# Kernel optimization log

Hardware: AMD Instinct MI355X
Metric: run time of the kernel (lower is better)

Reference implementation:

```python
import jax, jax.numpy as jnp
import numpy as np

B = 8192          # number of ragged samples (lengths.numel())
T = 1048576       # total tokens = sum(lengths), static for jit
NTOKEN = 100000
NHID = 256
NCLASSES = 14


def setup_inputs() -> dict:
    key = jax.random.key(0)
    k1, k2, k3, k4, k5 = jax.random.split(key, 5)
    # ragged lengths summing exactly to T: diff of sorted cut points
    cuts = jnp.sort(jax.random.randint(k1, (B - 1,), 0, T))
    bounds = jnp.concatenate([jnp.array([0], dtype=cuts.dtype), cuts,
                              jnp.array([T], dtype=cuts.dtype)])
    lengths = (bounds[1:] - bounds[:-1]).astype(jnp.int64)  # [B], may contain 0
    indices = jax.random.randint(k2, (T,), 0, NTOKEN).astype(jnp.int64)
    emb = jax.random.normal(k3, (NTOKEN, NHID), dtype=jnp.float32)
    W = jax.random.normal(k4, (NHID, NCLASSES), dtype=jnp.float32) / jnp.sqrt(jnp.float32(NHID))
    b = jax.random.normal(k5, (NCLASSES,), dtype=jnp.float32) * 0.01
    return {"lengths": lengths, "indices": indices, "emb": emb, "W": W, "b": b}


def reference(lengths, indices, emb, W, b):
    # segment id for each flat token: sample i owns lengths[i] consecutive tokens
    seg = jnp.repeat(jnp.arange(B), lengths, total_repeat_length=T)  # [T]
    gathered = emb[indices]                                          # [T, NHID]
    sums = jax.ops.segment_sum(gathered, seg, num_segments=B)       # [B, NHID]
    len_f = lengths.astype(sums.dtype)[:, None]                      # [B, 1]
    means = jnp.where(len_f > 0, sums / jnp.maximum(len_f, 1), 0.0)  # zero rows for empty samples
    return jnp.tanh(means) @ W + b                                   # [B, NCLASSES]
```

## Files before the change

kernel.cpp:

```cpp
#include <hip/hip_runtime.h>

#define B_SAMPLES 8192
#define NHID 256
#define NCLASSES 14
#define T_TOKENS 1048576
#define CHUNK 128
#define NWAVES (T_TOKENS / CHUNK)
#define NTOKEN_ROWS 100000
#define LMIN 40
#define SUMS_OFFSET 65536
#define SUMS_BYTES ((size_t)B_SAMPLES * NHID * 4)
#define EMB8_OFFSET (SUMS_OFFSET + SUMS_BYTES)
#define EMB8_BYTES ((size_t)NTOKEN_ROWS * NHID)
#define CONV_BLOCKS ((NTOKEN_ROWS * NHID) / (16 * 256))

__global__ __launch_bounds__(256) void scan_convert_kernel(
    const int* __restrict__ lengths, int* __restrict__ bounds,
    const float* __restrict__ emb, unsigned* __restrict__ emb8)
{
    if (blockIdx.x == 0) {
        __shared__ int s_sum[256];
        const int t = threadIdx.x;
        int local[32];
        int sum = 0;
#pragma unroll
        for (int k = 0; k < 32; ++k) {
            int v = lengths[t * 32 + k];
            local[k] = v;
            sum += v;
        }
        s_sum[t] = sum;
        __syncthreads();
        for (int off = 1; off < 256; off <<= 1) {
            int v = (t >= off) ? s_sum[t - off] : 0;
            __syncthreads();
            s_sum[t] += v;
            __syncthreads();
        }
        int run = (t > 0) ? s_sum[t - 1] : 0;
#pragma unroll
        for (int k = 0; k < 32; ++k) {
            bounds[t * 32 + k] = run;
            run += local[k];
        }
        if (t == 255) bounds[B_SAMPLES] = run;
    } else {
        const size_t i = ((size_t)(blockIdx.x - 1) * 256 + threadIdx.x) * 16;
        const float4 a = *reinterpret_cast<const float4*>(emb + i);
        const float4 b = *reinterpret_cast<const float4*>(emb + i + 4);
        const float4 c = *reinterpret_cast<const float4*>(emb + i + 8);
        const float4 d = *reinterpret_cast<const float4*>(emb + i + 12);
        uint4 o;
        int w;
        w = __builtin_amdgcn_cvt_pk_fp8_f32(a.x, a.y, 0, false);
        w = __builtin_amdgcn_cvt_pk_fp8_f32(a.z, a.w, w, true);
        o.x = (unsigned)w;
        w = __builtin_amdgcn_cvt_pk_fp8_f32(b.x, b.y, 0, false);
        w = __builtin_amdgcn_cvt_pk_fp8_f32(b.z, b.w, w, true);
        o.y = (unsigned)w;
        w = __builtin_amdgcn_cvt_pk_fp8_f32(c.x, c.y, 0, false);
        w = __builtin_amdgcn_cvt_pk_fp8_f32(c.z, c.w, w, true);
        o.z = (unsigned)w;
        w = __builtin_amdgcn_cvt_pk_fp8_f32(d.x, d.y, 0, false);
        w = __builtin_amdgcn_cvt_pk_fp8_f32(d.z, d.w, w, true);
        o.w = (unsigned)w;
        *reinterpret_cast<uint4*>(emb8 + i / 4) = o;
    }
}

#define FLUSH_ACC()                                                          \
    {                                                                        \
        float* dst_ = sums + (size_t)s * NHID + lane * 4;                    \
        if (inter) {                                                         \
            *reinterpret_cast<float4*>(dst_) = make_float4(ax, ay, az, aw);  \
        } else {                                                             \
            unsafeAtomicAdd(dst_ + 0, ax);                                   \
            unsafeAtomicAdd(dst_ + 1, ay);                                   \
            unsafeAtomicAdd(dst_ + 2, az);                                   \
            unsafeAtomicAdd(dst_ + 3, aw);                                   \
        }                                                                    \
    }

#define ACCUM(V, T_)                                                         \
    {                                                                        \
        if ((T_) == se) {                                                    \
            FLUSH_ACC();                                                     \
            ax = ay = az = aw = 0.f;                                         \
            ++s;                                                             \
            while (bounds[s + 1] <= (T_)) ++s;                               \
            se = bounds[s + 1];                                              \
            inter = (bounds[s] >= t0) && (se <= t1);                         \
        }                                                                    \
        {                                                                    \
            auto lo_ = __builtin_amdgcn_cvt_pk_f32_fp8((int)(V), false);     \
            auto hi_ = __builtin_amdgcn_cvt_pk_f32_fp8((int)(V), true);      \
            ax += lo_[0];                                                    \
            ay += lo_[1];                                                    \
            az += hi_[0];                                                    \
            aw += hi_[1];                                                    \
        }                                                                    \
    }

__global__ __launch_bounds__(256) void chunk_gather_fp8_kernel(
    const int* __restrict__ indices,
    const unsigned* __restrict__ emb8,
    const int* __restrict__ bounds,
    float* __restrict__ sums)
{
    const int wave = blockIdx.x * 4 + (threadIdx.x >> 6);
    const int lane = threadIdx.x & 63;
    const int t0 = wave * CHUNK;
    const int t1 = t0 + CHUNK;

    int lo = 0, hi = B_SAMPLES - 1;
    while (lo < hi) {
        const int mid = (lo + hi) >> 1;
        if (bounds[mid + 1] > t0) hi = mid; else lo = mid + 1;
    }
    int s = lo;
    int se = bounds[s + 1];
    bool inter = (bounds[s] >= t0) && (se <= t1);

    float ax = 0.f, ay = 0.f, az = 0.f, aw = 0.f;
    const int* ip = indices + t0;
    int4 ca = *reinterpret_cast<const int4*>(ip);
    int4 cb = *reinterpret_cast<const int4*>(ip + 4);

    for (int g = 0; g < CHUNK / 8; ++g) {
        int4 na = ca, nb = cb;
        if (g + 1 < CHUNK / 8) {
            na = *reinterpret_cast<const int4*>(ip + 8);
            nb = *reinterpret_cast<const int4*>(ip + 12);
        }
        ip += 8;
        const unsigned v0 = emb8[(size_t)(unsigned)ca.x * (NHID / 4) + lane];
        const unsigned v1 = emb8[(size_t)(unsigned)ca.y * (NHID / 4) + lane];
        const unsigned v2 = emb8[(size_t)(unsigned)ca.z * (NHID / 4) + lane];
        const unsigned v3 = emb8[(size_t)(unsigned)ca.w * (NHID / 4) + lane];
        const unsigned v4 = emb8[(size_t)(unsigned)cb.x * (NHID / 4) + lane];
        const unsigned v5 = emb8[(size_t)(unsigned)cb.y * (NHID / 4) + lane];
        const unsigned v6 = emb8[(size_t)(unsigned)cb.z * (NHID / 4) + lane];
        const unsigned v7 = emb8[(size_t)(unsigned)cb.w * (NHID / 4) + lane];

        const int tb = t0 + g * 8;
        ACCUM(v0, tb + 0)
        ACCUM(v1, tb + 1)
        ACCUM(v2, tb + 2)
        ACCUM(v3, tb + 3)
        ACCUM(v4, tb + 4)
        ACCUM(v5, tb + 5)
        ACCUM(v6, tb + 6)
        ACCUM(v7, tb + 7)
        ca = na;
        cb = nb;
    }
    FLUSH_ACC();
}

__global__ __launch_bounds__(256, 8) void head_kernel(
    const float* __restrict__ sums,
    const int* __restrict__ bounds,
    const int* __restrict__ indices,
    const float* __restrict__ emb,
    const float* __restrict__ W,
    const float* __restrict__ bias,
    float* __restrict__ out)
{
    const int s = blockIdx.x * 4 + (threadIdx.x >> 6);
    const int lane = threadIdx.x & 63;
    const int start = bounds[s];
    const int len = bounds[s + 1] - start;

    float ax, ay, az, aw;
    if (len >= LMIN) {
        const float4 v = *reinterpret_cast<const float4*>(sums + (size_t)s * NHID + lane * 4);
        ax = v.x; ay = v.y; az = v.z; aw = v.w;
    } else {
        ax = ay = az = aw = 0.f;
        const int* ip = indices + start;
        int j = 0;
        for (; j + 4 <= len; j += 4) {
            const int r0 = ip[j + 0];
            const int r1 = ip[j + 1];
            const int r2 = ip[j + 2];
            const int r3 = ip[j + 3];
            const float4 v0 = *reinterpret_cast<const float4*>(emb + (size_t)r0 * NHID + lane * 4);
            const float4 v1 = *reinterpret_cast<const float4*>(emb + (size_t)r1 * NHID + lane * 4);
            const float4 v2 = *reinterpret_cast<const float4*>(emb + (size_t)r2 * NHID + lane * 4);
            const float4 v3 = *reinterpret_cast<const float4*>(emb + (size_t)r3 * NHID + lane * 4);
            ax += (v0.x + v1.x) + (v2.x + v3.x);
            ay += (v0.y + v1.y) + (v2.y + v3.y);
            az += (v0.z + v1.z) + (v2.z + v3.z);
            aw += (v0.w + v1.w) + (v2.w + v3.w);
        }
        for (; j < len; ++j) {
            const int r = ip[j];
            const float4 v = *reinterpret_cast<const float4*>(emb + (size_t)r * NHID + lane * 4);
            ax += v.x; ay += v.y; az += v.z; aw += v.w;
        }
    }

    const float inv = (len > 0) ? 1.f / (float)len : 0.f;
    float th[4];
    th[0] = tanhf(ax * inv);
    th[1] = tanhf(ay * inv);
    th[2] = tanhf(az * inv);
    th[3] = tanhf(aw * inv);

    float p[NCLASSES];
#pragma unroll
    for (int c = 0; c < NCLASSES; ++c) p[c] = 0.f;
#pragma unroll
    for (int k = 0; k < 4; ++k) {
        const float* wr = W + (size_t)(lane * 4 + k) * NCLASSES;
#pragma unroll
        for (int c = 0; c < NCLASSES; ++c) p[c] += th[k] * wr[c];
    }
#pragma unroll
    for (int c = 0; c < NCLASSES; ++c) {
#pragma unroll
        for (int off = 32; off > 0; off >>= 1) p[c] += __shfl_xor(p[c], off);
    }
    if (lane == 0) {
#pragma unroll
        for (int c = 0; c < NCLASSES; ++c)
            out[(size_t)s * NCLASSES + c] = p[c] + bias[c];
    }
}

__global__ __launch_bounds__(256, 8) void seg_mean_head_kernel(
    const int* __restrict__ indices,
    const float* __restrict__ emb,
    const float* __restrict__ W,
    const float* __restrict__ bias,
    const int* __restrict__ bounds,
    float* __restrict__ out)
{
    const int i = blockIdx.x;
    const int start = bounds[i];
    const int L = bounds[i + 1] - start;
    const int tid = threadIdx.x;
    const int sub = tid >> 6;
    const int lane = tid & 63;

    __shared__ int s_idx[256];
    __shared__ float s_red[4 * NHID];
    __shared__ float s_t[NHID];

    float ax = 0.f, ay = 0.f, az = 0.f, aw = 0.f;
    for (int t0 = 0; t0 < L; t0 += 256) {
        const int n = min(256, L - t0);
        __syncthreads();
        if (tid < n) s_idx[tid] = indices[start + t0 + tid];
        __syncthreads();
        int j = 0;
        for (; j + 8 <= n; j += 8) {
            const int r0 = s_idx[j + sub];
            const int r1 = s_idx[j + 4 + sub];
            const float4 v0 = *reinterpret_cast<const float4*>(emb + (size_t)r0 * NHID + lane * 4);
            const float4 v1 = *reinterpret_cast<const float4*>(emb + (size_t)r1 * NHID + lane * 4);
            ax += v0.x + v1.x; ay += v0.y + v1.y; az += v0.z + v1.z; aw += v0.w + v1.w;
        }
        for (; j < n; j += 4) {
            if (j + sub < n) {
                const int r = s_idx[j + sub];
                const float4 v = *reinterpret_cast<const float4*>(emb + (size_t)r * NHID + lane * 4);
                ax += v.x; ay += v.y; az += v.z; aw += v.w;
            }
        }
    }
    s_red[sub * NHID + lane * 4 + 0] = ax;
    s_red[sub * NHID + lane * 4 + 1] = ay;
    s_red[sub * NHID + lane * 4 + 2] = az;
    s_red[sub * NHID + lane * 4 + 3] = aw;
    __syncthreads();
    const float tot = s_red[0 * NHID + tid] + s_red[1 * NHID + tid] +
                      s_red[2 * NHID + tid] + s_red[3 * NHID + tid];
    const float mean = (L > 0) ? tot / (float)L : 0.f;
    s_t[tid] = tanhf(mean);
    __syncthreads();
    if (tid < 16 * NCLASSES) {
        const int c = tid >> 4;
        const int j = tid & 15;
        float p = 0.f;
#pragma unroll
        for (int k = 0; k < NHID / 16; ++k) {
            const int h = j + k * 16;
            p += s_t[h] * W[h * NCLASSES + c];
        }
#pragma unroll
        for (int off = 8; off > 0; off >>= 1) p += __shfl_down(p, off, 16);
        if (j == 0) out[(size_t)i * NCLASSES + c] = p + bias[c];
    }
}

__global__ __launch_bounds__(256) void scan_lengths_kernel(
    const int* __restrict__ lengths, int* __restrict__ bounds)
{
    __shared__ int s_sum[256];
    const int t = threadIdx.x;
    int local[32];
    int sum = 0;
#pragma unroll
    for (int k = 0; k < 32; ++k) {
        int v = lengths[t * 32 + k];
        local[k] = v;
        sum += v;
    }
    s_sum[t] = sum;
    __syncthreads();
    for (int off = 1; off < 256; off <<= 1) {
        int v = (t >= off) ? s_sum[t - off] : 0;
        __syncthreads();
        s_sum[t] += v;
        __syncthreads();
    }
    int run = (t > 0) ? s_sum[t - 1] : 0;
#pragma unroll
    for (int k = 0; k < 32; ++k) {
        bounds[t * 32 + k] = run;
        run += local[k];
    }
    if (t == 255) bounds[B_SAMPLES] = run;
}

extern "C" void kernel_launch(void* const* d_in, const int* in_sizes, int n_in,
                              void* d_out, int out_size, void* d_ws, size_t ws_size,
                              hipStream_t stream) {
    const int*   lengths = (const int*)d_in[0];
    const int*   indices = (const int*)d_in[1];
    const float* emb     = (const float*)d_in[2];
    const float* W       = (const float*)d_in[3];
    const float* bias    = (const float*)d_in[4];
    float*       out     = (float*)d_out;
    int*         bounds  = (int*)d_ws;

    if (ws_size >= EMB8_OFFSET + EMB8_BYTES) {
        float*    sums = (float*)((char*)d_ws + SUMS_OFFSET);
        unsigned* emb8 = (unsigned*)((char*)d_ws + EMB8_OFFSET);
        (void)hipMemsetAsync(sums, 0, SUMS_BYTES, stream);
        scan_convert_kernel<<<1 + CONV_BLOCKS, 256, 0, stream>>>(lengths, bounds, emb, emb8);
        chunk_gather_fp8_kernel<<<NWAVES / 4, 256, 0, stream>>>(indices, emb8, bounds, sums);
        head_kernel<<<B_SAMPLES / 4, 256, 0, stream>>>(sums, bounds, indices, emb, W, bias, out);
    } else {
        scan_lengths_kernel<<<1, 256, 0, stream>>>(lengths, bounds);
        seg_mean_head_kernel<<<B_SAMPLES, 256, 0, stream>>>(indices, emb, W, bias, bounds, out);
    }
}
```

Baseline: 110.8 us.

## Gather four tokens per wave with 16-byte fp8 loads and fold memset into scan

The gather kernel now splits each wave into four 16-lane groups, each loading a full 256-byte fp8 row as uint4 per lane, so one wave processes four tokens per step. Per-group partial sums are combined with cross-lane shuffles before being stored or atomically added. Indices are staged in shared memory and the row loads are prefetched through a small register ring. The separate memset of the sums buffer is replaced by extra zeroing blocks in the scan/convert kernel, which saves a launch. In exchange, the per-segment-boundary handling gets more complex and adds shuffle reductions at every flush.

```diff
diff --git a/kernel.cpp b/kernel.cpp
--- a/kernel.cpp
+++ b/kernel.cpp
@@ -5,6 +5,8 @@
 #define NCLASSES 14
 #define T_TOKENS 1048576
 #define CHUNK 128
+#define QUADS (CHUNK / 4)
+#define QD 4
 #define NWAVES (T_TOKENS / CHUNK)
 #define NTOKEN_ROWS 100000
 #define LMIN 40
@@ -13,12 +15,15 @@
 #define EMB8_OFFSET (SUMS_OFFSET + SUMS_BYTES)
 #define EMB8_BYTES ((size_t)NTOKEN_ROWS * NHID)
 #define CONV_BLOCKS ((NTOKEN_ROWS * NHID) / (16 * 256))
-
-__global__ __launch_bounds__(256) void scan_convert_kernel(
+#define ZERO_BLOCKS 512
+
+__global__ __launch_bounds__(256) void scan_convert_zero_kernel(
     const int* __restrict__ lengths, int* __restrict__ bounds,
-    const float* __restrict__ emb, unsigned* __restrict__ emb8)
-{
-    if (blockIdx.x == 0) {
+    const float* __restrict__ emb, unsigned* __restrict__ emb8,
+    float4* __restrict__ sums4)
+{
+    const int b = blockIdx.x;
+    if (b == 0) {
         __shared__ int s_sum[256];
         const int t = threadIdx.x;
         int local[32];
@@ -44,10 +49,10 @@
             run += local[k];
         }
         if (t == 255) bounds[B_SAMPLES] = run;
-    } else {
-        const size_t i = ((size_t)(blockIdx.x - 1) * 256 + threadIdx.x) * 16;
+    } else if (b <= CONV_BLOCKS) {
+        const size_t i = ((size_t)(b - 1) * 256 + threadIdx.x) * 16;
         const float4 a = *reinterpret_cast<const float4*>(emb + i);
-        const float4 b = *reinterpret_cast<const float4*>(emb + i + 4);
+        const float4 bb = *reinterpret_cast<const float4*>(emb + i + 4);
         const float4 c = *reinterpret_cast<const float4*>(emb + i + 8);
         const float4 d = *reinterpret_cast<const float4*>(emb + i + 12);
         uint4 o;
@@ -55,8 +60,8 @@
         w = __builtin_amdgcn_cvt_pk_fp8_f32(a.x, a.y, 0, false);
         w = __builtin_amdgcn_cvt_pk_fp8_f32(a.z, a.w, w, true);
         o.x = (unsigned)w;
-        w = __builtin_amdgcn_cvt_pk_fp8_f32(b.x, b.y, 0, false);
-        w = __builtin_amdgcn_cvt_pk_fp8_f32(b.z, b.w, w, true);
+        w = __builtin_amdgcn_cvt_pk_fp8_f32(bb.x, bb.y, 0, false);
+        w = __builtin_amdgcn_cvt_pk_fp8_f32(bb.z, bb.w, w, true);
         o.y = (unsigned)w;
         w = __builtin_amdgcn_cvt_pk_fp8_f32(c.x, c.y, 0, false);
         w = __builtin_amdgcn_cvt_pk_fp8_f32(c.z, c.w, w, true);
@@ -65,52 +70,90 @@
         w = __builtin_amdgcn_cvt_pk_fp8_f32(d.z, d.w, w, true);
         o.w = (unsigned)w;
         *reinterpret_cast<uint4*>(emb8 + i / 4) = o;
-    }
-}
-
-#define FLUSH_ACC()                                                          \
-    {                                                                        \
-        float* dst_ = sums + (size_t)s * NHID + lane * 4;                    \
-        if (inter) {                                                         \
-            *reinterpret_cast<float4*>(dst_) = make_float4(ax, ay, az, aw);  \
-        } else {                                                             \
-            unsafeAtomicAdd(dst_ + 0, ax);                                   \
-            unsafeAtomicAdd(dst_ + 1, ay);                                   \
-            unsafeAtomicAdd(dst_ + 2, az);                                   \
-            unsafeAtomicAdd(dst_ + 3, aw);                                   \
-        }                                                                    \
-    }
-
-#define ACCUM(V, T_)                                                         \
-    {                                                                        \
-        if ((T_) == se) {                                                    \
-            FLUSH_ACC();                                                     \
-            ax = ay = az = aw = 0.f;                                         \
-            ++s;                                                             \
-            while (bounds[s + 1] <= (T_)) ++s;                               \
-            se = bounds[s + 1];                                              \
-            inter = (bounds[s] >= t0) && (se <= t1);                         \
-        }                                                                    \
-        {                                                                    \
-            auto lo_ = __builtin_amdgcn_cvt_pk_f32_fp8((int)(V), false);     \
-            auto hi_ = __builtin_amdgcn_cvt_pk_f32_fp8((int)(V), true);      \
-            ax += lo_[0];                                                    \
-            ay += lo_[1];                                                    \
-            az += hi_[0];                                                    \
-            aw += hi_[1];                                                    \
-        }                                                                    \
-    }
-
-__global__ __launch_bounds__(256) void chunk_gather_fp8_kernel(
+    } else {
+        const int z = b - 1 - CONV_BLOCKS;
+        const float4 zer = make_float4(0.f, 0.f, 0.f, 0.f);
+        float4* p = sums4 + (size_t)z * 1024 + threadIdx.x;
+#pragma unroll
+        for (int k = 0; k < 4; ++k) p[k * 256] = zer;
+    }
+}
+
+
+#define ADD_ALL(V)                                                            \
+    {                                                                         \
+        { auto f_ = __builtin_amdgcn_cvt_pk_f32_fp8((int)(V).x, false); acc[0] += f_[0];  acc[1] += f_[1]; }  \
+        { auto f_ = __builtin_amdgcn_cvt_pk_f32_fp8((int)(V).x, true);  acc[2] += f_[0];  acc[3] += f_[1]; }  \
+        { auto f_ = __builtin_amdgcn_cvt_pk_f32_fp8((int)(V).y, false); acc[4] += f_[0];  acc[5] += f_[1]; }  \
+        { auto f_ = __builtin_amdgcn_cvt_pk_f32_fp8((int)(V).y, true);  acc[6] += f_[0];  acc[7] += f_[1]; }  \
+        { auto f_ = __builtin_amdgcn_cvt_pk_f32_fp8((int)(V).z, false); acc[8] += f_[0];  acc[9] += f_[1]; }  \
+        { auto f_ = __builtin_amdgcn_cvt_pk_f32_fp8((int)(V).z, true);  acc[10] += f_[0]; acc[11] += f_[1]; } \
+        { auto f_ = __builtin_amdgcn_cvt_pk_f32_fp8((int)(V).w, false); acc[12] += f_[0]; acc[13] += f_[1]; } \
+        { auto f_ = __builtin_amdgcn_cvt_pk_f32_fp8((int)(V).w, true);  acc[14] += f_[0]; acc[15] += f_[1]; } \
+    }
+
+#define FLUSHQ()                                                              \
+    {                                                                         \
+        float r_[16];                                                         \
+        _Pragma("unroll") for (int j_ = 0; j_ < 16; ++j_) {                   \
+            float t_ = acc[j_];                                               \
+            t_ += __shfl_xor(t_, 16);                                         \
+            t_ += __shfl_xor(t_, 32);                                         \
+            r_[j_] = t_;                                                      \
+        }                                                                     \
+        if (grp == 0) {                                                       \
+            float* dst_ = sums + (size_t)s * NHID + sub * 16;                 \
+            if (inter) {                                                      \
+                *reinterpret_cast<float4*>(dst_ + 0)  = make_float4(r_[0],  r_[1],  r_[2],  r_[3]);  \
+                *reinterpret_cast<float4*>(dst_ + 4)  = make_float4(r_[4],  r_[5],  r_[6],  r_[7]);  \
+                *reinterpret_cast<float4*>(dst_ + 8)  = make_float4(r_[8],  r_[9],  r_[10], r_[11]); \
+                *reinterpret_cast<float4*>(dst_ + 12) = make_float4(r_[12], r_[13], r_[14], r_[15]); \
+            } else {                                                          \
+                _Pragma("unroll") for (int j_ = 0; j_ < 16; ++j_)             \
+                    unsafeAtomicAdd(dst_ + j_, r_[j_]);                       \
+            }                                                                 \
+        }                                                                     \
+    }
+
+#define CONSUME(V, TB)                                                        \
+    {                                                                         \
+        if (se > (TB) + 3) {                                                  \
+            ADD_ALL(V)                                                        \
+        } else {                                                              \
+            bool pend = true;                                                 \
+            while (se <= (TB) + 3) {                                          \
+                if (pend && ((TB) + grp < se)) { ADD_ALL(V) pend = false; }   \
+                FLUSHQ();                                                     \
+                _Pragma("unroll") for (int j_ = 0; j_ < 16; ++j_) acc[j_] = 0.f; \
+                const int ose_ = se;                                          \
+                do { ++s; } while (bounds[s + 1] <= ose_);                    \
+                se = bounds[s + 1];                                           \
+                inter = (bounds[s] >= t0) && (se <= t1);                      \
+            }                                                                 \
+            if (pend) { ADD_ALL(V) }                                          \
+        }                                                                     \
+    }
+
+__global__ __launch_bounds__(256) void chunk_gather_fp8q_kernel(
     const int* __restrict__ indices,
-    const unsigned* __restrict__ emb8,
+    const uint4* __restrict__ emb8q,
     const int* __restrict__ bounds,
     float* __restrict__ sums)
 {
-    const int wave = blockIdx.x * 4 + (threadIdx.x >> 6);
-    const int lane = threadIdx.x & 63;
-    const int t0 = wave * CHUNK;
+    __shared__ int s_idx[512];
+    const int tid = threadIdx.x;
+    const int bt0 = blockIdx.x * 512;
+    s_idx[tid] = indices[bt0 + tid];
+    s_idx[tid + 256] = indices[bt0 + 256 + tid];
+    __syncthreads();
+
+    const int wv = tid >> 6;
+    const int lane = tid & 63;
+    const int grp = lane >> 4;
+    const int sub = lane & 15;
+    const int t0 = bt0 + wv * CHUNK;
     const int t1 = t0 + CHUNK;
+    const int* wip = s_idx + wv * CHUNK;
 
     int lo = 0, hi = B_SAMPLES - 1;
     while (lo < hi) {
@@ -121,40 +164,35 @@
     int se = bounds[s + 1];
     bool inter = (bounds[s] >= t0) && (se <= t1);
 
-    float ax = 0.f, ay = 0.f, az = 0.f, aw = 0.f;
-    const int* ip = indices + t0;
-    int4 ca = *reinterpret_cast<const int4*>(ip);
-    int4 cb = *reinterpret_cast<const int4*>(ip + 4);
-
-    for (int g = 0; g < CHUNK / 8; ++g) {
-        int4 na = ca, nb = cb;
-        if (g + 1 < CHUNK / 8) {
-            na = *reinterpret_cast<const int4*>(ip + 8);
-            nb = *reinterpret_cast<const int4*>(ip + 12);
-        }
-        ip += 8;
-        const unsigned v0 = emb8[(size_t)(unsigned)ca.x * (NHID / 4) + lane];
-        const unsigned v1 = emb8[(size_t)(unsigned)ca.y * (NHID / 4) + lane];
-        const unsigned v2 = emb8[(size_t)(unsigned)ca.z * (NHID / 4) + lane];
-        const unsigned v3 = emb8[(size_t)(unsigned)ca.w * (NHID / 4) + lane];
-        const unsigned v4 = emb8[(size_t)(unsigned)cb.x * (NHID / 4) + lane];
-        const unsigned v5 = emb8[(size_t)(unsigned)cb.y * (NHID / 4) + lane];
-        const unsigned v6 = emb8[(size_t)(unsigned)cb.z * (NHID / 4) + lane];
-        const unsigned v7 = emb8[(size_t)(unsigned)cb.w * (NHID / 4) + lane];
-
-        const int tb = t0 + g * 8;
-        ACCUM(v0, tb + 0)
-        ACCUM(v1, tb + 1)
-        ACCUM(v2, tb + 2)
-        ACCUM(v3, tb + 3)
-        ACCUM(v4, tb + 4)
-        ACCUM(v5, tb + 5)
-        ACCUM(v6, tb + 6)
-        ACCUM(v7, tb + 7)
-        ca = na;
-        cb = nb;
-    }
-    FLUSH_ACC();
+    float acc[16];
+#pragma unroll
+    for (int j = 0; j < 16; ++j) acc[j] = 0.f;
+
+    uint4 vbuf[QD];
+#pragma unroll
+    for (int q = 0; q < QD; ++q) {
+        const unsigned r = (unsigned)wip[4 * q + grp];
+        vbuf[q] = emb8q[(size_t)r * (NHID / 16) + sub];
+    }
+    int rnext = wip[4 * QD + grp];
+
+#pragma unroll 4
+    for (int q = 0; q < QUADS - QD; ++q) {
+        const uint4 v = vbuf[q & (QD - 1)];
+        const int rcur = rnext;
+        const int nq = q + QD + 1;
+        rnext = wip[(nq < QUADS ? nq * 4 : 0) + grp];
+        vbuf[q & (QD - 1)] = emb8q[(size_t)(unsigned)rcur * (NHID / 16) + sub];
+        const int tb = t0 + q * 4;
+        CONSUME(v, tb)
+    }
+#pragma unroll
+    for (int q = QUADS - QD; q < QUADS; ++q) {
+        const uint4 v = vbuf[q & (QD - 1)];
+        const int tb = t0 + q * 4;
+        CONSUME(v, tb)
+    }
+    FLUSHQ();
 }
 
 __global__ __launch_bounds__(256, 8) void head_kernel(
@@ -338,9 +376,10 @@
     if (ws_size >= EMB8_OFFSET + EMB8_BYTES) {
         float*    sums = (float*)((char*)d_ws + SUMS_OFFSET);
         unsigned* emb8 = (unsigned*)((char*)d_ws + EMB8_OFFSET);
-        (void)hipMemsetAsync(sums, 0, SUMS_BYTES, stream);
-        scan_convert_kernel<<<1 + CONV_BLOCKS, 256, 0, stream>>>(lengths, bounds, emb, emb8);
-        chunk_gather_fp8_kernel<<<NWAVES / 4, 256, 0, stream>>>(indices, emb8, bounds, sums);
+        scan_convert_zero_kernel<<<1 + CONV_BLOCKS + ZERO_BLOCKS, 256, 0, stream>>>(
+            lengths, bounds, emb, emb8, (float4*)sums);
+        chunk_gather_fp8q_kernel<<<NWAVES / 4, 256, 0, stream>>>(
+            indices, (const uint4*)emb8, bounds, sums);
         head_kernel<<<B_SAMPLES / 4, 256, 0, stream>>>(sums, bounds, indices, emb, W, bias, out);
     } else {
         scan_lengths_kernel<<<1, 256, 0, stream>>>(lengths, bounds);
```

Result: slower. 274.9 us (+148.1%).
